# Kernel optimization log

Measured on AMD Instinct MI355X. Metric: run time of the kernel, lower is better.

## Reference

```python
import jax, jax.numpy as jnp
import numpy as np
from jax import lax

S = 16  # encoder stride (patchify-conv stand-in for the CNN backbone, stride-16 feature grid)


def _conv(x, w, b, stride, padding):
    y = lax.conv_general_dilated(x, w, (stride, stride), padding,
                                 dimension_numbers=('NCHW', 'OIHW', 'NCHW'))
    return y + b[None, :, None, None]


def _l2norm(x, eps=1e-12):  # F.normalize(p=2, dim=1)
    n = jnp.sqrt(jnp.sum(x * x, axis=1, keepdims=True))
    return x / jnp.maximum(n, eps)


def _encode(frame, ew, eb, kw, kb, vw, vb, mask=None):
    feat = jax.nn.relu(_conv(frame, ew, eb, S, 'VALID'))  # [B,512,h,w]
    key = _conv(feat, kw, kb, 1, 'SAME')                  # [B,64,h,w]
    val = _conv(feat, vw, vb, 1, 'SAME')                  # [B,ed,h,w]
    if mask is not None:
        m = mask[:, None, ::S, ::S]  # torch F.interpolate 'nearest' with exact integer factor
        key = key * m
        val = val * m
    return _l2norm(key), val, feat


def _forward(query_frame, prev_frame, prev_mask, first_frame, first_mask,
             enc_q_w, enc_q_b, enc_m_w, enc_m_b,
             key_w, key_b, val_w, val_b,
             dec1_w, dec1_b, dec2_w, dec2_b, cls_w, cls_b):
    # memory bank reset + push(first), push(prev)
    k1, v1, _ = _encode(first_frame, enc_m_w, enc_m_b, key_w, key_b, val_w, val_b, first_mask)
    kp, vp, _ = _encode(prev_frame, enc_m_w, enc_m_b, key_w, key_b, val_w, val_b, prev_mask)
    qk, qv, _ = _encode(query_frame, enc_q_w, enc_q_b, key_w, key_b, val_w, val_b)
    B, Ck, h, w = qk.shape
    ed = qv.shape[1]
    mem_key = jnp.concatenate([k1.reshape(B, Ck, -1), kp.reshape(B, Ck, -1)], axis=2)  # [B,64,M]
    mem_val = jnp.concatenate([v1.reshape(B, ed, -1), vp.reshape(B, ed, -1)], axis=2)  # [B,ed,M]
    q_key = qk.reshape(B, Ck, -1)                                                      # [B,64,Q]
    # STM memory read: affinity -> softmax -> weighted sum over memory pixels
    affinity = jnp.einsum('bcq,bcm->bqm', q_key, mem_key) / jnp.sqrt(jnp.float32(Ck))
    affinity = jax.nn.softmax(affinity, axis=-1)
    mem_read = jnp.einsum('bqm,bcm->bcq', affinity, mem_val).reshape(B, ed, h, w)
    fused = jnp.concatenate([qv, mem_read], axis=1)  # [B,2*ed,h,w] (aspp=False)
    d = jax.nn.relu(_conv(fused, dec1_w, dec1_b, 1, 'SAME'))
    dec_feat = jax.nn.relu(_conv(d, dec2_w, dec2_b, 1, 'SAME'))
    logits = _conv(dec_feat, cls_w, cls_b, 1, 'SAME')
    H, W = query_frame.shape[-2], query_frame.shape[-1]
    logits_full = jax.image.resize(logits, (B, logits.shape[1], H, W), method='bilinear')  # align_corners=False
    rep_feat = _l2norm(dec_feat)
    return rep_feat, logits_full


def setup_inputs():
    key = jax.random.key(0)
    ks = jax.random.split(key, 16)
    B, H, W = 8, 512, 512
    Ce, Ck, ed = 512, 64, 256
    g = lambda i, sh, s: jax.random.normal(ks[i], sh, dtype=jnp.float32) * s
    return {
        'query_frame': g(0, (B, 3, H, W), 1.0),
        'prev_frame': g(1, (B, 3, H, W), 1.0),
        'prev_mask': jnp.round(jax.random.uniform(ks[2], (B, H, W), dtype=jnp.float32)),
        'first_frame': g(3, (B, 3, H, W), 1.0),
        'first_mask': jnp.round(jax.random.uniform(ks[4], (B, H, W), dtype=jnp.float32)),
        'enc_q_w': g(5, (Ce, 3, S, S), 0.02), 'enc_q_b': jnp.zeros((Ce,), jnp.float32),
        'enc_m_w': g(6, (Ce, 3, S, S), 0.02), 'enc_m_b': jnp.zeros((Ce,), jnp.float32),
        'key_w': g(7, (Ck, Ce, 1, 1), 0.05), 'key_b': jnp.zeros((Ck,), jnp.float32),
        'val_w': g(8, (ed, Ce, 1, 1), 0.05), 'val_b': jnp.zeros((ed,), jnp.float32),
        'dec1_w': g(9, (ed, 2 * ed, 3, 3), 0.02), 'dec1_b': jnp.zeros((ed,), jnp.float32),
        'dec2_w': g(10, (ed, ed, 3, 3), 0.02), 'dec2_b': jnp.zeros((ed,), jnp.float32),
        'cls_w': g(11, (2, ed, 1, 1), 0.05), 'cls_b': jnp.zeros((2,), jnp.float32),
    }


def reference(query_frame, prev_frame, prev_mask, first_frame, first_mask,
              enc_q_w, enc_q_b, enc_m_w, enc_m_b,
              key_w, key_b, val_w, val_b,
              dec1_w, dec1_b, dec2_w, dec2_b, cls_w, cls_b):
    return _forward(query_frame, prev_frame, prev_mask, first_frame, first_mask,
                    enc_q_w, enc_q_b, enc_m_w, enc_m_b,
                    key_w, key_b, val_w, val_b,
                    dec1_w, dec1_b, dec2_w, dec2_b, cls_w, cls_b)
```

## Files before the change

### kernel.cpp

```cpp
#include <hip/hip_runtime.h>
#include <hip/hip_bf16.h>
#include <cstdint>

#define DEV __device__ __forceinline__
typedef __attribute__((ext_vector_type(8))) short short8;
typedef __attribute__((ext_vector_type(4))) float f32x4;
typedef unsigned short u16;

DEV float b2f(u16 u) { union { unsigned int i; float f; } x; x.i = (unsigned)u << 16; return x.f; }
DEV u16 f2b(float f) { __hip_bfloat16 h = __float2bfloat16(f); return *(u16*)&h; }
DEV float rdin(const void* p, size_t i, int isbf) {
  return isbf ? __bfloat162float(((const __hip_bfloat16*)p)[i]) : ((const float*)p)[i];
}
DEV void wrout(void* p, size_t i, float v, int isbf) {
  if (isbf) ((__hip_bfloat16*)p)[i] = __float2bfloat16(v);
  else      ((float*)p)[i] = v;
}
DEV short8 ld8(const void* p, size_t idx, int isbf) {
  if (isbf) return *(const short8*)((const u16*)p + idx);
  const float* f = (const float*)p + idx;
  float4 x = *(const float4*)f, y = *(const float4*)(f + 4);
  short8 r;
  r[0] = f2b(x.x); r[1] = f2b(x.y); r[2] = f2b(x.z); r[3] = f2b(x.w);
  r[4] = f2b(y.x); r[5] = f2b(y.y); r[6] = f2b(y.z); r[7] = f2b(y.w);
  return r;
}
DEV void gl16(const u16* g, u16* l) {
  __builtin_amdgcn_global_load_lds(
      (const __attribute__((address_space(1))) void*)g,
      (__attribute__((address_space(3))) void*)l, 16, 0, 0);
}
DEV void bar() {
  asm volatile("" ::: "memory");
  __builtin_amdgcn_s_barrier();
  asm volatile("" ::: "memory");
}

__global__ __launch_bounds__(256) void detect_k(const u16* w, int* flag) {
  __shared__ int cnt[256];
  int tid = threadIdx.x, c = 0;
  for (int i = tid; i < 4096; i += 256) {
    u16 v = w[i];
    int e = (v >> 7) & 0xFF;
    if (v == 0 || (e >= 0x60 && e <= 0x9F)) c++;
  }
  cnt[tid] = c;
  __syncthreads();
  for (int s = 128; s > 0; s >>= 1) { if (tid < s) cnt[tid] += cnt[tid + s]; __syncthreads(); }
  if (tid == 0) *flag = (cnt[0] > 3600) ? 1 : 0;
}

__global__ __launch_bounds__(256) void patchify_k(const void* F0, const void* F1,
                                                  u16* dst, const int* dflag) {
  int isbf = *dflag;
  int bid = blockIdx.x;
  int z = bid >> 8, rem = bid & 255, b = rem >> 5, y = rem & 31;
  const void* F = z ? F1 : F0;
  int x = threadIdx.x & 31, pj = threadIdx.x >> 5;
  u16* drow = dst + (size_t)(z * 8192 + b * 1024 + y * 32 + x) * 768;
#pragma unroll
  for (int i = 0; i < 6; i++) {
    int pair = i * 8 + pj;
    int c = pair >> 4, ky = pair & 15;
    size_t src = ((size_t)((b * 3 + c) * 512 + y * 16 + ky)) * 512 + x * 16;
    short8 v0 = ld8(F, src, isbf);
    short8 v1 = ld8(F, src + 8, isbf);
    u16* dp = drow + c * 256 + ky * 16;
    *(short8*)dp = v0;
    *(short8*)(dp + 8) = v1;
  }
}

__global__ __launch_bounds__(256) void wconv_k(const void* wm, const void* wq,
                                               u16* dst, const int* dflag) {
  int isbf = *dflag;
  int gi = blockIdx.x * 256 + threadIdx.x;
  size_t e0 = (size_t)gi * 8;
  const void* src = e0 < 393216 ? wm : wq;
  size_t off = e0 < 393216 ? e0 : e0 - 393216;
  *(short8*)&dst[e0] = ld8(src, off, isbf);
}

__global__ __launch_bounds__(256) void kvconv_k(const void* valW, const void* keyW,
                                                u16* dst, const int* dflag) {
  int isbf = *dflag;
  int idx = blockIdx.x * 256 + threadIdx.x;
  size_t e0 = (size_t)idx * 8;
  int row = (int)(e0 >> 9);
  const void* src = row < 256 ? valW : keyW;
  size_t off = row < 256 ? e0 : e0 - (size_t)256 * 512;
  *(short8*)&dst[e0] = ld8(src, off, isbf);
}

struct PA {
  const void* W0; const void* W1; size_t bs; int K; int rowsplit; int zsel; int ws16; int rowmax1;
  DEV short8 l8(int row, int k, int b, int zz, int isbf) const {
    const void* W = W0; int r = row;
    if (zsel && zz == 2) W = W1;
    else if (rowsplit && row >= rowsplit) { W = W1; r = row - rowsplit; if (r > rowmax1) r = rowmax1; }
    return ld8(W, (size_t)b * bs + (size_t)r * K + k, ws16 ? 1 : isbf);
  }
  DEV const u16* ga(int row, int k, int b, int zz) const {
    int r = row; if (rowsplit && r > rowmax1) r = rowmax1;
    return (const u16*)W0 + (size_t)b * bs + (size_t)r * K + k;
  }
};
struct PBws {
  const u16* X; int rs; size_t zs;
  DEV short8 l8(int t, int k, int zz, int) const {
    return *(const short8*)(X + (size_t)zz * zs + (size_t)t * rs + k);
  }
  DEV const u16* ga(int t, int k, int zz) const {
    return X + (size_t)zz * zs + (size_t)t * rs + k;
  }
};
struct PBc3 {
  const u16* X; int C; int shift;
  DEV short8 l8(int t, int k, int, int) const {
    int tap = k >> shift, c0 = k & (C - 1);
    int dy = tap / 3, dx = tap - dy * 3;
    int pos = t & 1023, y = pos >> 5, x = pos & 31;
    int iy = y + dy - 1, ix = x + dx - 1;
    if ((unsigned)iy >= 32u || (unsigned)ix >= 32u) { short8 z = {0,0,0,0,0,0,0,0}; return z; }
    return *(const short8*)(X + (size_t)(((t >> 10) * 1024) + iy * 32 + ix) * C + c0);
  }
};

struct Epi {
  int mode;
  u16 *o16, *o16b, *o16c;
  size_t zs; int ts, moff, mmax;
  const void *bias, *bias2; int bzsel;
  const void *maskA, *maskB;
  const float* rscale;
  float scale; int relu, doexp;
  DEV void store1(int m, int t, int z, float v, int isbf) const {
    if (m >= mmax) return;
    int b = t >> 10, pos = t & 1023;
    if (m < 256) {
      v += rdin(bias, m, isbf);
      if (z < 2) {
        const void* mk = z ? maskB : maskA;
        v *= rdin(mk, ((size_t)(b * 512 + (pos >> 5) * 16) << 9) + (pos & 31) * 16, isbf);
        o16[((size_t)(b * 256 + m)) * 2048 + (size_t)z * 1024 + pos] = f2b(v);
      } else {
        o16b[(size_t)t * 512 + m] = f2b(v);
      }
    } else {
      v += rdin(bias2, m - 256, isbf);
      o16c[((size_t)z * 8192 + t) * 64 + (m - 256)] = f2b(v);
    }
  }
};

DEV void epilogue(const Epi& ep, f32x4 (&acc)[4][4], u16* sh, int isbf, int tid,
                  int col16, int quad, int wm, int wn, int zz, int m0, int n0, int nbase) {
  if (ep.mode == 1) {
#pragma unroll
    for (int mt = 0; mt < 4; mt++)
#pragma unroll
      for (int nt = 0; nt < 4; nt++)
#pragma unroll
        for (int r = 0; r < 4; r++) {
          int m = m0 + wm * 64 + mt * 16 + quad * 4 + r;
          int t = nbase + n0 + wn * 64 + nt * 16 + col16;
          ep.store1(m, t, zz, acc[mt][nt][r], isbf);
        }
    return;
  }
  if (ep.mode == 2) {
    float* pf = (float*)ep.o16;
#pragma unroll
    for (int mt = 0; mt < 4; mt++)
#pragma unroll
      for (int nt = 0; nt < 4; nt++)
#pragma unroll
        for (int r = 0; r < 4; r++) {
          int m = m0 + wm * 64 + mt * 16 + quad * 4 + r;
          int t = nbase + n0 + wn * 64 + nt * 16 + col16;
          pf[((size_t)(zz * 256 + m)) * 8192 + t] = acc[mt][nt][r];
        }
    return;
  }
  u16* T = sh;
  const int TS = 132;
  for (int p = 0; p < 2; p++) {
    __syncthreads();
    if (wn == p) {
#pragma unroll
      for (int mt = 0; mt < 4; mt++)
#pragma unroll
        for (int nt = 0; nt < 4; nt++) {
          int tl = nt * 16 + col16;
#pragma unroll
          for (int r2 = 0; r2 < 2; r2++) {
            int ml = wm * 64 + mt * 16 + quad * 4 + r2 * 2;
            float v0 = acc[mt][nt][r2 * 2] * ep.scale;
            float v1 = acc[mt][nt][r2 * 2 + 1] * ep.scale;
            if (ep.bias) {
              const void* bp = (ep.bzsel && zz == 2) ? ep.bias2 : ep.bias;
              v0 += rdin(bp, m0 + ml, isbf);
              v1 += rdin(bp, m0 + ml + 1, isbf);
            }
            if (ep.relu) { v0 = fmaxf(v0, 0.f); v1 = fmaxf(v1, 0.f); }
            unsigned int pk = (unsigned)f2b(v0) | ((unsigned)f2b(v1) << 16);
            *(unsigned int*)&T[tl * TS + ml] = pk;
          }
        }
    }
    __syncthreads();
    {
      int tl = tid >> 2, seg = tid & 3;
      int tg = nbase + n0 + p * 64 + tl;
      u16* op = ep.o16 + (size_t)zz * ep.zs + (size_t)tg * ep.ts + ep.moff + m0;
#pragma unroll
      for (int i = 0; i < 4; i++) {
        int c8 = seg + i * 4;
        short8 v = *(short8*)&T[tl * TS + c8 * 8];
        *(short8*)&op[c8 * 8] = v;
      }
    }
  }
}

template <class PB>
__global__ __launch_bounds__(256) void mgl(PA pa, PB pb, Epi ep, int ktiles, int nbase,
                                           const int* dflag) {
  __shared__ u16 sh[32768];
  int isbf = *dflag;
  int tid = threadIdx.x, lane = tid & 63;
  int col16 = lane & 15, quad = lane >> 4;
  int wv = tid >> 6, wm = wv >> 1, wn = wv & 1;
  int zz = blockIdx.z;
  int n0 = blockIdx.x * 128, m0 = blockIdx.y * 128;
  int bA = (nbase + n0) >> 10;

  f32x4 acc[4][4];
#pragma unroll
  for (int mt = 0; mt < 4; mt++)
#pragma unroll
    for (int nt = 0; nt < 4; nt++)
#pragma unroll
      for (int r = 0; r < 4; r++) acc[mt][nt][r] = 0.f;

  int rA[4], lA[4];
#pragma unroll
  for (int g = 0; g < 4; g++) {
    rA[g] = g * 32 + (tid >> 3);
    lA[g] = (tid & 7) ^ (rA[g] & 7);
  }

  auto issue = [&](int kt) {
    int kk = kt * 64;
    u16* base = sh + ((kt & 1) << 14);
#pragma unroll
    for (int g = 0; g < 4; g++) {
      gl16(pa.ga(m0 + rA[g], kk + lA[g] * 8, bA, zz), base + (size_t)(g * 256 + tid) * 8);
      gl16(pb.ga(nbase + n0 + rA[g], kk + lA[g] * 8, zz), base + 8192 + (size_t)(g * 256 + tid) * 8);
    }
  };
  issue(0);

  for (int kt = 0; kt < ktiles; kt++) {
    const u16* As = sh + ((kt & 1) << 14);
    const u16* Bs = As + 8192;
    if (kt + 1 < ktiles) {
      issue(kt + 1);
      asm volatile("s_waitcnt vmcnt(8)" ::: "memory");
    } else {
      asm volatile("s_waitcnt vmcnt(0)" ::: "memory");
    }
    bar();
#pragma unroll
    for (int s = 0; s < 2; s++) {
      short8 af[4], bf[4];
      int cs = ((s * 4 + quad) ^ (col16 & 7)) << 3;
#pragma unroll
      for (int mt = 0; mt < 4; mt++)
        af[mt] = *(const short8*)&As[(wm * 64 + mt * 16 + col16) * 64 + cs];
#pragma unroll
      for (int nt = 0; nt < 4; nt++)
        bf[nt] = *(const short8*)&Bs[(wn * 64 + nt * 16 + col16) * 64 + cs];
#pragma unroll
      for (int mt = 0; mt < 4; mt++)
#pragma unroll
        for (int nt = 0; nt < 4; nt++)
          acc[mt][nt] = __builtin_amdgcn_mfma_f32_16x16x32_bf16(af[mt], bf[nt], acc[mt][nt], 0, 0, 0);
    }
    bar();
  }

  epilogue(ep, acc, sh, isbf, tid, col16, quad, wm, wn, zz, m0, n0, nbase);
}

template <class PB>
__global__ __launch_bounds__(256) void mg(PA pa, PB pb, Epi ep, int ktiles, int nbase,
                                          int ksplit, const int* dflag) {
  __shared__ u16 sh[32768];
  int isbf = *dflag;
  int tid = threadIdx.x, lane = tid & 63;
  int col16 = lane & 15, quad = lane >> 4;
  int wv = tid >> 6, wm = wv >> 1, wn = wv & 1;
  int zz = blockIdx.z;
  int kb = ksplit * zz;
  int n0 = blockIdx.x * 128, m0 = blockIdx.y * 128;
  int bA = (nbase + n0) >> 10;

  f32x4 acc[4][4];
#pragma unroll
  for (int mt = 0; mt < 4; mt++)
#pragma unroll
    for (int nt = 0; nt < 4; nt++)
#pragma unroll
      for (int r = 0; r < 4; r++) acc[mt][nt][r] = 0.f;

  int rA[4], lA[4];
#pragma unroll
  for (int g = 0; g < 4; g++) {
    rA[g] = g * 32 + (tid >> 3);
    lA[g] = (tid & 7) ^ (rA[g] & 7);
  }

  short8 ra[4], rb[4];
#pragma unroll
  for (int g = 0; g < 4; g++) {
    ra[g] = pa.l8(m0 + rA[g], kb + lA[g] * 8, bA, zz, isbf);
    rb[g] = pb.l8(nbase + n0 + rA[g], kb + lA[g] * 8, zz, isbf);
  }
#pragma unroll
  for (int g = 0; g < 4; g++) {
    *(short8*)&sh[(size_t)(g * 256 + tid) * 8] = ra[g];
    *(short8*)&sh[8192 + (size_t)(g * 256 + tid) * 8] = rb[g];
  }
  __syncthreads();

  for (int kt = 0; kt < ktiles; kt++) {
    const u16* As = sh + ((kt & 1) ? 16384 : 0);
    const u16* Bs = As + 8192;
    bool more = (kt + 1 < ktiles);
    if (more) {
      int kn = kb + (kt + 1) * 64;
#pragma unroll
      for (int g = 0; g < 4; g++) {
        ra[g] = pa.l8(m0 + rA[g], kn + lA[g] * 8, bA, zz, isbf);
        rb[g] = pb.l8(nbase + n0 + rA[g], kn + lA[g] * 8, zz, isbf);
      }
    }
#pragma unroll
    for (int s = 0; s < 2; s++) {
      short8 af[4], bf[4];
      int cs = ((s * 4 + quad) ^ (col16 & 7)) << 3;
#pragma unroll
      for (int mt = 0; mt < 4; mt++)
        af[mt] = *(const short8*)&As[(wm * 64 + mt * 16 + col16) * 64 + cs];
#pragma unroll
      for (int nt = 0; nt < 4; nt++)
        bf[nt] = *(const short8*)&Bs[(wn * 64 + nt * 16 + col16) * 64 + cs];
#pragma unroll
      for (int mt = 0; mt < 4; mt++)
#pragma unroll
        for (int nt = 0; nt < 4; nt++)
          acc[mt][nt] = __builtin_amdgcn_mfma_f32_16x16x32_bf16(af[mt], bf[nt], acc[mt][nt], 0, 0, 0);
    }
    if (more) {
      u16* An = sh + (!(kt & 1) ? 16384 : 0);
#pragma unroll
      for (int g = 0; g < 4; g++) {
        *(short8*)&An[(size_t)(g * 256 + tid) * 8] = ra[g];
        *(short8*)&An[8192 + (size_t)(g * 256 + tid) * 8] = rb[g];
      }
      __syncthreads();
    }
  }

  epilogue(ep, acc, sh, isbf, tid, col16, quad, wm, wn, zz, m0, n0, nbase);
}

__global__ __launch_bounds__(256) void attn_k(const u16* qk, const u16* memk,
                                              const u16* memv, float* pf, float* rsum) {
  __shared__ u16 sh[28672];
  __shared__ float rsl[4][64];
  const int Qt = 0, Kt = 4096, Vt = 8192, Pl = 24576;
  int tid = threadIdx.x, lane = tid & 63;
  int col16 = lane & 15, quad = lane >> 4;
  int wv = tid >> 6;
  int xl = blockIdx.x;
  int x = ((xl & 7) << 4) | (xl >> 3);
  int b = x >> 4, qt = x & 15;
  int q0 = b * 1024 + qt * 64;
  int s = blockIdx.y;
  int kv0 = s * 512;

  rsl[wv][lane] = 0.f;

  int r32 = tid >> 3;
#pragma unroll
  for (int g = 0; g < 2; g++) {
    int row = g * 32 + r32;
    int k8 = (tid & 7) ^ (row & 7);
    gl16(qk + (size_t)(q0 + row) * 64 + k8 * 8, sh + Qt + (size_t)(g * 256 + tid) * 8);
  }
  {
#pragma unroll
    for (int g = 0; g < 2; g++) {
      int row = g * 32 + r32;
      int k8 = (tid & 7) ^ (row & 7);
      gl16(memk + ((size_t)(b * 2048 + kv0 + row)) * 64 + k8 * 8,
           sh + Kt + (size_t)(g * 256 + tid) * 8);
    }
#pragma unroll
    for (int g = 0; g < 8; g++) {
      int row = g * 32 + r32;
      int k8 = (tid & 7) ^ (row & 7);
      gl16(memv + ((size_t)(b * 256 + row)) * 2048 + kv0 + k8 * 8,
           sh + Vt + (size_t)(g * 256 + tid) * 8);
    }
  }
  __syncthreads();

  f32x4 acc_o[4][4];
#pragma unroll
  for (int mt = 0; mt < 4; mt++)
#pragma unroll
    for (int nt = 0; nt < 4; nt++)
#pragma unroll
      for (int r = 0; r < 4; r++) acc_o[mt][nt][r] = 0.f;

  for (int ch = 0; ch < 8; ch++) {
    {
      f32x4 acc_s[4];
#pragma unroll
      for (int nt = 0; nt < 4; nt++)
#pragma unroll
        for (int r = 0; r < 4; r++) acc_s[nt][r] = 0.f;
#pragma unroll
      for (int s2 = 0; s2 < 2; s2++) {
        int cs = ((s2 * 4 + quad) ^ (col16 & 7)) << 3;
        short8 af = *(const short8*)&sh[Kt + (wv * 16 + col16) * 64 + cs];
        short8 bf[4];
#pragma unroll
        for (int nt = 0; nt < 4; nt++)
          bf[nt] = *(const short8*)&sh[Qt + (nt * 16 + col16) * 64 + cs];
#pragma unroll
        for (int nt = 0; nt < 4; nt++)
          acc_s[nt] = __builtin_amdgcn_mfma_f32_16x16x32_bf16(af, bf[nt], acc_s[nt], 0, 0, 0);
      }
#pragma unroll
      for (int nt = 0; nt < 4; nt++) {
        int ql = nt * 16 + col16;
        float tsum = 0.f;
#pragma unroll
        for (int r = 0; r < 4; r++) {
          int kvl = wv * 16 + quad * 4 + r;
          u16 pb = f2b(__expf(0.125f * acc_s[nt][r]));
          tsum += b2f(pb);
          sh[Pl + ql * 64 + (((kvl >> 3) ^ (ql & 7)) << 3) + (kvl & 7)] = pb;
        }
        tsum += __shfl_xor(tsum, 16);
        tsum += __shfl_xor(tsum, 32);
        if (quad == 0) rsl[wv][ql] += tsum;
      }
    }
    __syncthreads();
    if (ch + 1 < 8) {
      int kvc = kv0 + (ch + 1) * 64;
#pragma unroll
      for (int g = 0; g < 2; g++) {
        int row = g * 32 + r32;
        int k8 = (tid & 7) ^ (row & 7);
        gl16(memk + ((size_t)(b * 2048 + kvc + row)) * 64 + k8 * 8,
             sh + Kt + (size_t)(g * 256 + tid) * 8);
      }
    }
#pragma unroll
    for (int s2 = 0; s2 < 2; s2++) {
      short8 af[4], bf[4];
      int cs = ((s2 * 4 + quad) ^ (col16 & 7)) << 3;
#pragma unroll
      for (int mt = 0; mt < 4; mt++)
        af[mt] = *(const short8*)&sh[Vt + (wv * 64 + mt * 16 + col16) * 64 + cs];
#pragma unroll
      for (int nt = 0; nt < 4; nt++)
        bf[nt] = *(const short8*)&sh[Pl + (nt * 16 + col16) * 64 + cs];
#pragma unroll
      for (int mt = 0; mt < 4; mt++)
#pragma unroll
        for (int nt = 0; nt < 4; nt++)
          acc_o[mt][nt] = __builtin_amdgcn_mfma_f32_16x16x32_bf16(af[mt], bf[nt], acc_o[mt][nt], 0, 0, 0);
    }
    __syncthreads();
    if (ch + 1 < 8) {
      int kvc = kv0 + (ch + 1) * 64;
#pragma unroll
      for (int g = 0; g < 8; g++) {
        int row = g * 32 + r32;
        int k8 = (tid & 7) ^ (row & 7);
        gl16(memv + ((size_t)(b * 256 + row)) * 2048 + kvc + k8 * 8,
             sh + Vt + (size_t)(g * 256 + tid) * 8);
      }
    }
    __syncthreads();
  }

#pragma unroll
  for (int mt = 0; mt < 4; mt++)
#pragma unroll
    for (int nt = 0; nt < 4; nt++)
#pragma unroll
      for (int r = 0; r < 4; r++) {
        int c = wv * 64 + mt * 16 + quad * 4 + r;
        int q = nt * 16 + col16;
        pf[((size_t)(s * 8192 + q0 + q)) * 256 + c] = acc_o[mt][nt][r];
      }
  if (tid < 64)
    atomicAdd(&rsum[q0 + tid], rsl[0][tid] + rsl[1][tid] + rsl[2][tid] + rsl[3][tid]);
}

__global__ __launch_bounds__(256) void acomb_k(const float* pf, const float* rsum,
                                               u16* fused) {
  int tid = threadIdx.x;
  int t = blockIdx.x * 2 + (tid >> 7);
  int cp = tid & 127;
  float inv = 1.f / rsum[t];
  float v0 = 0.f, v1 = 0.f;
#pragma unroll
  for (int s = 0; s < 4; s++) {
    const float* p = pf + ((size_t)(s * 8192 + t)) * 256 + cp * 2;
    v0 += p[0]; v1 += p[1];
  }
  unsigned int pk = (unsigned)f2b(v0 * inv) | ((unsigned)f2b(v1 * inv) << 16);
  *(unsigned int*)&fused[(size_t)t * 512 + 256 + cp * 2] = pk;
}

__global__ __launch_bounds__(256) void comb_k(const float* pf, const void* bias,
                                              u16* out, int ts, int moff, int npart,
                                              int relu, const int* dflag) {
  int isbf = *dflag;
  int tid = threadIdx.x;
  int t = blockIdx.x * 64 + (tid & 63);
  int m = blockIdx.y * 8 + ((tid >> 6) << 1);
  float v0 = 0.f, v1 = 0.f;
  for (int p = 0; p < npart; p++) {
    v0 += pf[(size_t)(p * 256 + m) * 8192 + t];
    v1 += pf[(size_t)(p * 256 + m + 1) * 8192 + t];
  }
  if (bias) { v0 += rdin(bias, m, isbf); v1 += rdin(bias, m + 1, isbf); }
  if (relu) { v0 = fmaxf(v0, 0.f); v1 = fmaxf(v1, 0.f); }
  unsigned int pk = (unsigned)f2b(v0) | ((unsigned)f2b(v1) << 16);
  *(unsigned int*)&out[(size_t)t * ts + moff + m] = pk;
}

__global__ __launch_bounds__(256) void wreorder_k(const void* src, u16* dst, int C,
                                                  int total, const int* dflag) {
  int idx = blockIdx.x * 256 + threadIdx.x;
  if (idx >= total) return;
  int isbf = *dflag;
  int nine_c = 9 * C;
  int m = idx / nine_c; int r = idx - m * nine_c;
  int tp = r / C; int c = r - tp * C;
  dst[idx] = f2b(rdin(src, (size_t)(m * C + c) * 9 + tp, isbf));
}

__global__ __launch_bounds__(256) void keyfix_k(const u16* kraw3, const void* mA,
                                                const void* mB, u16* memk, u16* qk,
                                                float* rsum, const int* dflag) {
  int isbf = *dflag;
  int z = blockIdx.y;
  int n = blockIdx.x * 256 + threadIdx.x;
  int b = n >> 10, pos = n & 1023;
  if (z == 0) rsum[n] = 0.f;
  float mv = 1.f;
  if (z == 0) mv = rdin(mA, ((size_t)(b * 512 + (pos >> 5) * 16) << 9) + (pos & 31) * 16, isbf);
  else if (z == 1) mv = rdin(mB, ((size_t)(b * 512 + (pos >> 5) * 16) << 9) + (pos & 31) * 16, isbf);
  const u16* src = kraw3 + ((size_t)z * 8192 + n) * 64;
  float v[64], ss = 0.f;
#pragma unroll
  for (int c = 0; c < 64; c++) { v[c] = b2f(src[c]) * mv; ss += v[c] * v[c]; }
  float inv = 1.f / fmaxf(sqrtf(ss), 1e-12f);
  u16* dst = (z < 2) ? memk + (size_t)(b * 2048 + z * 1024 + pos) * 64 : qk + (size_t)n * 64;
#pragma unroll
  for (int c = 0; c < 64; c++) dst[c] = f2b(v[c] * inv);
}

__global__ __launch_bounds__(256) void repcls_k(const u16* decf, const void* cwgt,
                                                const void* cbias, void* out_rep,
                                                float* logits, const int* dflag) {
  int isbf = *dflag;
  int tid = threadIdx.x, lane = tid & 63, wv = tid >> 6;
  int tok = blockIdx.x * 4 + wv;
  int b = tok >> 10, pos = tok & 1023;
  const u16* src = decf + (size_t)tok * 256;
  int c0 = lane * 4;
  float v[4], ss = 0.f, a0 = 0.f, a1 = 0.f;
#pragma unroll
  for (int j = 0; j < 4; j++) {
    float x = b2f(src[c0 + j]);
    v[j] = x; ss += x * x;
    a0 = fmaf(x, rdin(cwgt, c0 + j, isbf), a0);
    a1 = fmaf(x, rdin(cwgt, 256 + c0 + j, isbf), a1);
  }
#pragma unroll
  for (int off = 32; off > 0; off >>= 1) {
    ss += __shfl_down(ss, off); a0 += __shfl_down(a0, off); a1 += __shfl_down(a1, off);
  }
  ss = __shfl(ss, 0); a0 = __shfl(a0, 0); a1 = __shfl(a1, 0);
  float inv = 1.f / fmaxf(sqrtf(ss), 1e-12f);
#pragma unroll
  for (int j = 0; j < 4; j++)
    wrout(out_rep, ((size_t)(b * 256 + c0 + j) << 10) + pos, v[j] * inv, isbf);
  if (lane == 0) {
    logits[((size_t)(b * 2) << 10) + pos]     = a0 + rdin(cbias, 0, isbf);
    logits[((size_t)(b * 2 + 1) << 10) + pos] = a1 + rdin(cbias, 1, isbf);
  }
}

__global__ __launch_bounds__(256) void resize_k(const float* logits, void* out,
                                                size_t ebase, const int* dflag) {
  int isbf = *dflag;
  int idx = blockIdx.x * 256 + threadIdx.x;
  int ox = idx & 511, oy = (idx >> 9) & 511, c = (idx >> 18) & 1, b = idx >> 19;
  float fy = (oy + 0.5f) * 0.0625f - 0.5f;
  float fx = (ox + 0.5f) * 0.0625f - 0.5f;
  int y0 = (int)floorf(fy), x0 = (int)floorf(fx);
  float wy = fy - y0, wx = fx - x0;
  int y0c = max(y0, 0), y1c = min(y0 + 1, 31);
  int x0c = max(x0, 0), x1c = min(x0 + 1, 31);
  const float* L = logits + ((size_t)(b * 2 + c) << 10);
  float v00 = L[y0c * 32 + x0c], v01 = L[y0c * 32 + x1c];
  float v10 = L[y1c * 32 + x0c], v11 = L[y1c * 32 + x1c];
  float v = (1.f - wy) * ((1.f - wx) * v00 + wx * v01) + wy * ((1.f - wx) * v10 + wx * v11);
  wrout(out, ebase + (size_t)idx, v, isbf);
}

extern "C" void kernel_launch(void* const* d_in, const int* in_sizes, int n_in,
                              void* d_out, int out_size, void* d_ws, size_t ws_size,
                              hipStream_t stream) {
  const void* query  = d_in[0];  const void* prev   = d_in[1];
  const void* prevM  = d_in[2];  const void* first  = d_in[3];
  const void* firstM = d_in[4];  const void* encQw  = d_in[5];
  const void* encQb  = d_in[6];  const void* encMw  = d_in[7];
  const void* encMb  = d_in[8];  const void* keyW   = d_in[9];
  const void* keyB   = d_in[10]; const void* valW   = d_in[11];
  const void* valB   = d_in[12]; const void* dec1W  = d_in[13];
  const void* dec1B  = d_in[14]; const void* dec2W  = d_in[15];
  const void* dec2B  = d_in[16]; const void* clsW   = d_in[17];
  const void* clsB   = d_in[18];

  u16* W = (u16*)d_ws;
  int* dflag = (int*)W;
  float* rsum   = (float*)(W + 16);
  float* logits = (float*)(W + 16400);
  u16* B0 = W + 49168;
  u16* Xp    = B0;
  u16* feat3 = B0 + 12582912;
  u16* encWb = B0 + 25165824;
  u16* wr1   = B0;
  u16* wr2   = B0 + 1179648;
  u16* fused = B0 + 1769472;
  u16* memv  = B0 + 5963776;
  u16* memk  = B0 + 10158080;
  u16* qk    = B0 + 11206656;
  u16* kraw3 = B0 + 25165824;
  u16* kvW   = B0 + 26738688;
  float* pf  = (float*)(B0 + 11730944);
  u16* dbuf  = memv;
  u16* decf  = memv + 2097152;

  dim3 blk(256);
  detect_k<<<dim3(1), blk, 0, stream>>>((const u16*)encQw, dflag);

  wconv_k<<<dim3(384), blk, 0, stream>>>(encMw, encQw, encWb, dflag);
  patchify_k<<<dim3(512), blk, 0, stream>>>(first, prev, Xp, dflag);
  {
    PA a{encWb, 0, 0, 768, 0, 0, 1, 0};
    PBws b{Xp, 768, (size_t)8192 * 768};
    Epi e{0, feat3, 0, 0, (size_t)8192 * 512, 512, 0, 512,
          encMb, 0, 0, 0, 0, 0, 1.f, 1, 0};
    mgl<PBws><<<dim3(64, 4, 2), blk, 0, stream>>>(a, b, e, 12, 0, dflag);
  }
  patchify_k<<<dim3(256), blk, 0, stream>>>(query, query, Xp, dflag);
  {
    PA a{encWb + 393216, 0, 0, 768, 0, 0, 1, 0};
    PBws b{Xp, 768, 0};
    Epi e{0, feat3 + (size_t)2 * 8192 * 512, 0, 0, 0, 512, 0, 512,
          encQb, 0, 0, 0, 0, 0, 1.f, 1, 0};
    mgl<PBws><<<dim3(64, 4, 1), blk, 0, stream>>>(a, b, e, 12, 0, dflag);
  }

  wreorder_k<<<dim3(4608), blk, 0, stream>>>(dec1W, wr1, 512, 256 * 4608, dflag);
  wreorder_k<<<dim3(2304), blk, 0, stream>>>(dec2W, wr2, 256, 256 * 2304, dflag);
  kvconv_k<<<dim3(80), blk, 0, stream>>>(valW, keyW, kvW, dflag);

  {
    PA a{kvW, 0, 0, 512, 1, 0, 1, 319};
    PBws b{feat3, 512, (size_t)8192 * 512};
    Epi e{1, memv, fused, kraw3, 0, 0, 0, 320,
          valB, keyB, 0, firstM, prevM, 0, 1.f, 0, 0};
    mgl<PBws><<<dim3(64, 3, 3), blk, 0, stream>>>(a, b, e, 8, 0, dflag);
  }
  keyfix_k<<<dim3(32, 3), blk, 0, stream>>>(kraw3, firstM, prevM, memk, qk, rsum, dflag);

  attn_k<<<dim3(128, 4), blk, 0, stream>>>(qk, memk, memv, pf, rsum);
  acomb_k<<<dim3(4096), blk, 0, stream>>>(pf, rsum, fused);

  {
    PA a{wr1, 0, 0, 4608, 0, 0, 1, 0};
    PBc3 b{fused, 512, 9};
    Epi e{2, (u16*)pf, 0, 0, 0, 0, 0, 0,
          0, 0, 0, 0, 0, 0, 1.f, 0, 0};
    mg<PBc3><<<dim3(64, 2, 4), blk, 0, stream>>>(a, b, e, 18, 0, 1152, dflag);
    comb_k<<<dim3(128, 32), blk, 0, stream>>>(pf, dec1B, dbuf, 256, 0, 4, 1, dflag);
  }
  {
    PA a{wr2, 0, 0, 2304, 0, 0, 1, 0};
    PBc3 b{dbuf, 256, 8};
    Epi e{2, (u16*)pf, 0, 0, 0, 0, 0, 0,
          0, 0, 0, 0, 0, 0, 1.f, 0, 0};
    mg<PBc3><<<dim3(64, 2, 2), blk, 0, stream>>>(a, b, e, 18, 0, 1152, dflag);
    comb_k<<<dim3(128, 32), blk, 0, stream>>>(pf, dec2B, decf, 256, 0, 2, 1, dflag);
  }

  repcls_k<<<dim3(2048), blk, 0, stream>>>(decf, clsW, clsB, d_out, logits, dflag);
  resize_k<<<dim3(16384), blk, 0, stream>>>(logits, d_out, (size_t)2097152, dflag);
}
```

Baseline: 441.8 us.

## Merge prep kernels, vectorize keyfix I/O, and widen dec2 split-K

Merges the weight conversion and patchify launches into one prep kernel, and folds the two weight reorders and the key/value weight conversion into a second. This removes several small launches and the gaps between them. keyfix now loads and stores keys as 8-wide bf16 vectors instead of scalar accesses. The dec2 conv GEMM is split four ways along K instead of two, which adds blocks but also more partial sums for comb_k to reduce.

After: 434.7 us. Within noise of the previous version (-1.6%).

```diff
diff --git a/kernel.cpp b/kernel.cpp
--- a/kernel.cpp
+++ b/kernel.cpp
@@ -50,46 +50,77 @@
   if (tid == 0) *flag = (cnt[0] > 3600) ? 1 : 0;
 }
 
-__global__ __launch_bounds__(256) void patchify_k(const void* F0, const void* F1,
-                                                  u16* dst, const int* dflag) {
+__global__ __launch_bounds__(256) void prep1_k(const void* F0, const void* F1,
+                                               u16* Xp, const void* wm, const void* wq,
+                                               u16* encWb, const int* dflag) {
   int isbf = *dflag;
   int bid = blockIdx.x;
-  int z = bid >> 8, rem = bid & 255, b = rem >> 5, y = rem & 31;
-  const void* F = z ? F1 : F0;
+  if (bid < 512) {
+    int z = bid >> 8, rem = bid & 255, b = rem >> 5, y = rem & 31;
+    const void* F = z ? F1 : F0;
+    int x = threadIdx.x & 31, pj = threadIdx.x >> 5;
+    u16* drow = Xp + (size_t)(z * 8192 + b * 1024 + y * 32 + x) * 768;
+#pragma unroll
+    for (int i = 0; i < 6; i++) {
+      int pair = i * 8 + pj;
+      int c = pair >> 4, ky = pair & 15;
+      size_t src = ((size_t)((b * 3 + c) * 512 + y * 16 + ky)) * 512 + x * 16;
+      short8 v0 = ld8(F, src, isbf);
+      short8 v1 = ld8(F, src + 8, isbf);
+      u16* dp = drow + c * 256 + ky * 16;
+      *(short8*)dp = v0;
+      *(short8*)(dp + 8) = v1;
+    }
+  } else {
+    int gi = (bid - 512) * 256 + threadIdx.x;
+    size_t e0 = (size_t)gi * 8;
+    const void* src = e0 < 393216 ? wm : wq;
+    size_t off = e0 < 393216 ? e0 : e0 - 393216;
+    *(short8*)&encWb[e0] = ld8(src, off, isbf);
+  }
+}
+
+__global__ __launch_bounds__(256) void patchify_k(const void* F0, u16* dst,
+                                                  const int* dflag) {
+  int isbf = *dflag;
+  int rem = blockIdx.x, b = rem >> 5, y = rem & 31;
   int x = threadIdx.x & 31, pj = threadIdx.x >> 5;
-  u16* drow = dst + (size_t)(z * 8192 + b * 1024 + y * 32 + x) * 768;
+  u16* drow = dst + (size_t)(b * 1024 + y * 32 + x) * 768;
 #pragma unroll
   for (int i = 0; i < 6; i++) {
     int pair = i * 8 + pj;
     int c = pair >> 4, ky = pair & 15;
     size_t src = ((size_t)((b * 3 + c) * 512 + y * 16 + ky)) * 512 + x * 16;
-    short8 v0 = ld8(F, src, isbf);
-    short8 v1 = ld8(F, src + 8, isbf);
+    short8 v0 = ld8(F0, src, isbf);
+    short8 v1 = ld8(F0, src + 8, isbf);
     u16* dp = drow + c * 256 + ky * 16;
     *(short8*)dp = v0;
     *(short8*)(dp + 8) = v1;
   }
 }
 
-__global__ __launch_bounds__(256) void wconv_k(const void* wm, const void* wq,
-                                               u16* dst, const int* dflag) {
-  int isbf = *dflag;
-  int gi = blockIdx.x * 256 + threadIdx.x;
-  size_t e0 = (size_t)gi * 8;
-  const void* src = e0 < 393216 ? wm : wq;
-  size_t off = e0 < 393216 ? e0 : e0 - 393216;
-  *(short8*)&dst[e0] = ld8(src, off, isbf);
-}
-
-__global__ __launch_bounds__(256) void kvconv_k(const void* valW, const void* keyW,
-                                                u16* dst, const int* dflag) {
-  int isbf = *dflag;
-  int idx = blockIdx.x * 256 + threadIdx.x;
-  size_t e0 = (size_t)idx * 8;
-  int row = (int)(e0 >> 9);
-  const void* src = row < 256 ? valW : keyW;
-  size_t off = row < 256 ? e0 : e0 - (size_t)256 * 512;
-  *(short8*)&dst[e0] = ld8(src, off, isbf);
+__global__ __launch_bounds__(256) void prep2_k(const void* dec1W, u16* wr1,
+                                               const void* dec2W, u16* wr2,
+                                               const void* valW, const void* keyW,
+                                               u16* kvW, const int* dflag) {
+  int isbf = *dflag;
+  int bid = blockIdx.x;
+  if (bid < 6912) {
+    const void* src; u16* dst; int C; int idx;
+    if (bid < 4608) { src = dec1W; dst = wr1; C = 512; idx = bid * 256 + threadIdx.x; }
+    else            { src = dec2W; dst = wr2; C = 256; idx = (bid - 4608) * 256 + threadIdx.x; }
+    int nine_c = 9 * C;
+    int m = idx / nine_c; int r = idx - m * nine_c;
+    int tp = r / C; int c = r - tp * C;
+    dst[idx] = f2b(rdin(src, (size_t)(m * C + c) * 9 + tp, isbf));
+  } else {
+    int idx = (bid - 6912) * 256 + threadIdx.x;
+    size_t e0 = (size_t)idx * 8;
+    int row = (int)(e0 >> 9);
+    const void* src = row < 256 ? valW : keyW;
+    size_t off = row < 256 ? e0 : e0 - (size_t)256 * 512;
+    *(short8*)&kvW[e0] = ld8(src, off, isbf);
+  }
 }
 
 struct PA {
@@ -550,17 +581,6 @@
   *(unsigned int*)&out[(size_t)t * ts + moff + m] = pk;
 }
 
-__global__ __launch_bounds__(256) void wreorder_k(const void* src, u16* dst, int C,
-                                                  int total, const int* dflag) {
-  int idx = blockIdx.x * 256 + threadIdx.x;
-  if (idx >= total) return;
-  int isbf = *dflag;
-  int nine_c = 9 * C;
-  int m = idx / nine_c; int r = idx - m * nine_c;
-  int tp = r / C; int c = r - tp * C;
-  dst[idx] = f2b(rdin(src, (size_t)(m * C + c) * 9 + tp, isbf));
-}
-
 __global__ __launch_bounds__(256) void keyfix_k(const u16* kraw3, const void* mA,
                                                 const void* mB, u16* memk, u16* qk,
                                                 float* rsum, const int* dflag) {
@@ -575,11 +595,23 @@
   const u16* src = kraw3 + ((size_t)z * 8192 + n) * 64;
   float v[64], ss = 0.f;
 #pragma unroll
-  for (int c = 0; c < 64; c++) { v[c] = b2f(src[c]) * mv; ss += v[c] * v[c]; }
+  for (int c8 = 0; c8 < 8; c8++) {
+    short8 xv = *(const short8*)(src + c8 * 8);
+#pragma unroll
+    for (int j = 0; j < 8; j++) {
+      float f = b2f((u16)xv[j]) * mv;
+      v[c8 * 8 + j] = f; ss += f * f;
+    }
+  }
   float inv = 1.f / fmaxf(sqrtf(ss), 1e-12f);
   u16* dst = (z < 2) ? memk + (size_t)(b * 2048 + z * 1024 + pos) * 64 : qk + (size_t)n * 64;
 #pragma unroll
-  for (int c = 0; c < 64; c++) dst[c] = f2b(v[c] * inv);
+  for (int c8 = 0; c8 < 8; c8++) {
+    short8 o;
+#pragma unroll
+    for (int j = 0; j < 8; j++) o[j] = f2b(v[c8 * 8 + j] * inv);
+    *(short8*)(dst + c8 * 8) = o;
+  }
 }
 
 __global__ __launch_bounds__(256) void repcls_k(const u16* decf, const void* cwgt,
@@ -669,8 +701,7 @@
   dim3 blk(256);
   detect_k<<<dim3(1), blk, 0, stream>>>((const u16*)encQw, dflag);
 
-  wconv_k<<<dim3(384), blk, 0, stream>>>(encMw, encQw, encWb, dflag);
-  patchify_k<<<dim3(512), blk, 0, stream>>>(first, prev, Xp, dflag);
+  prep1_k<<<dim3(896), blk, 0, stream>>>(first, prev, Xp, encMw, encQw, encWb, dflag);
   {
     PA a{encWb, 0, 0, 768, 0, 0, 1, 0};
     PBws b{Xp, 768, (size_t)8192 * 768};
@@ -678,7 +709,7 @@
           encMb, 0, 0, 0, 0, 0, 1.f, 1, 0};
     mgl<PBws><<<dim3(64, 4, 2), blk, 0, stream>>>(a, b, e, 12, 0, dflag);
   }
-  patchify_k<<<dim3(256), blk, 0, stream>>>(query, query, Xp, dflag);
+  patchify_k<<<dim3(256), blk, 0, stream>>>(query, Xp, dflag);
   {
     PA a{encWb + 393216, 0, 0, 768, 0, 0, 1, 0};
     PBws b{Xp, 768, 0};
@@ -687,9 +718,7 @@
     mgl<PBws><<<dim3(64, 4, 1), blk, 0, stream>>>(a, b, e, 12, 0, dflag);
   }
 
-  wreorder_k<<<dim3(4608), blk, 0, stream>>>(dec1W, wr1, 512, 256 * 4608, dflag);
-  wreorder_k<<<dim3(2304), blk, 0, stream>>>(dec2W, wr2, 256, 256 * 2304, dflag);
-  kvconv_k<<<dim3(80), blk, 0, stream>>>(valW, keyW, kvW, dflag);
+  prep2_k<<<dim3(6992), blk, 0, stream>>>(dec1W, wr1, dec2W, wr2, valW, keyW, kvW, dflag);
 
   {
     PA a{kvW, 0, 0, 512, 1, 0, 1, 319};
@@ -716,8 +745,8 @@
     PBc3 b{dbuf, 256, 8};
     Epi e{2, (u16*)pf, 0, 0, 0, 0, 0, 0,
           0, 0, 0, 0, 0, 0, 1.f, 0, 0};
-    mg<PBc3><<<dim3(64, 2, 2), blk, 0, stream>>>(a, b, e, 18, 0, 1152, dflag);
-    comb_k<<<dim3(128, 32), blk, 0, stream>>>(pf, dec2B, decf, 256, 0, 2, 1, dflag);
+    mg<PBc3><<<dim3(64, 2, 4), blk, 0, stream>>>(a, b, e, 9, 0, 576, dflag);
+    comb_k<<<dim3(128, 32), blk, 0, stream>>>(pf, dec2B, decf, 256, 0, 4, 1, dflag);
   }
 
   repcls_k<<<dim3(2048), blk, 0, stream>>>(decf, clsW, clsB, d_out, logits, dflag);
```
